# Performance work log

Measured on AMD Instinct MI355X. Metric: run time of the kernel, lower is better.

Reference implementation:

```python
import jax, jax.numpy as jnp
import numpy as np

N_HEAD = 8
D_MODEL = 512


def setup_inputs() -> dict:
    key = jax.random.key(0)
    ks = jax.random.split(key, 9)
    B, S, D, H = 4, 1024, D_MODEL, N_HEAD
    s = 1.0 / np.sqrt(D)
    return {
        "x": jax.random.normal(ks[0], (B, S, D), dtype=jnp.float32),
        "Wq": jax.random.normal(ks[1], (D, H * D), dtype=jnp.float32) * s,
        "bq": jnp.zeros((H * D,), jnp.float32),
        "Wk": jax.random.normal(ks[2], (D, H * D), dtype=jnp.float32) * s,
        "bk": jnp.zeros((H * D,), jnp.float32),
        "Wv": jax.random.normal(ks[3], (D, H * D), dtype=jnp.float32) * s,
        "bv": jnp.zeros((H * D,), jnp.float32),
        "Wo": jax.random.normal(ks[4], (H * D, D), dtype=jnp.float32) * (1.0 / np.sqrt(H * D)),
        "bo": jnp.zeros((D,), jnp.float32),
    }


def reference(x, Wq, bq, Wk, bk, Wv, bv, Wo, bo):
    B, S, D = x.shape
    H = N_HEAD
    # QKV projections, split into heads: [B, S, H, D] (each head uses full d_model)
    q = (x @ Wq + bq).reshape(B, S, H, D)
    k = (x @ Wk + bk).reshape(B, S, H, D)
    v = (x @ Wv + bv).reshape(B, S, H, D)
    # scores: [H, B, Sq, Sk], scaled by 1/d_model (scale=d_model in original)
    scores = jnp.einsum("bqhd,bkhd->hbqk", q, k) / D
    attn = jax.nn.softmax(scores, axis=-1)
    # context: [B, Sq, H, D] -> concat heads -> output projection
    ctx = jnp.einsum("hbqk,bkhd->bqhd", attn, v).reshape(B, S, H * D)
    out = ctx @ Wo + bo
    # attn returned as [(H*B), Sq, Sk] matching torch head-major layout
    return out, attn.reshape(H * B, S, S)
```

## Files before the change

### kernel.cpp

```cpp
#include <hip/hip_runtime.h>
#include <hip/hip_bf16.h>


typedef unsigned short u16;
typedef __attribute__((ext_vector_type(8))) short short8;
typedef __attribute__((ext_vector_type(4))) float f32x4;
typedef __attribute__((ext_vector_type(2))) unsigned int u32x2;

#define BK 32

__device__ __forceinline__ u16 f2bf(float f) {
    union { float f; unsigned u; } v; v.f = f;
    unsigned u = v.u;
    u += 0x7fffu + ((u >> 16) & 1u);
    return (u16)(u >> 16);
}

__device__ __forceinline__ void gl2lds16(const void* g, void* l) {
    __builtin_amdgcn_global_load_lds(
        (const __attribute__((address_space(1))) void*)g,
        (__attribute__((address_space(3))) void*)l, 16, 0, 0);
}

template<int MF, int NF, bool AF32, bool OUTF32, bool ROWBIAS, bool PIPE, bool DUALN>
__global__ __launch_bounds__(256, 4)
void gemm_bt(const void* __restrict__ Ap, int lda, long long sAh, long long sAb,
             const u16* __restrict__ Bp, int ldb, long long sBh, long long sBb,
             void* __restrict__ Cp, int ldc, long long sCh, long long sCb,
             int K, const float* __restrict__ bias, long long sbias,
             float scale, int nb,
             int nsplit, void* __restrict__ Cp2, const float* __restrict__ bias2)
{
    static_assert(!(PIPE && AF32), "PIPE path assumes bf16 A staging");
    constexpr int BMt = MF * 32, BNt = NF * 32;
    constexpr int AW = AF32 ? 2 * BK : BK;
    constexpr int NBUF = PIPE ? 3 : 1;
    constexpr int LPT = BMt / 64 + BNt / 64;
    __shared__ __attribute__((aligned(16))) u16 Alds[NBUF][BMt][AW];
    __shared__ __attribute__((aligned(16))) u16 Blds[NBUF][BNt][BK];

    int bx = blockIdx.x, by = blockIdx.y, bz = blockIdx.z;
    {
        const int gx = gridDim.x, gy = gridDim.y;
        const int nwg = gx * gy * (int)gridDim.z;
        const int wgid = bx + gx * (by + gy * bz);
        const int xcd = wgid & 7, lp = wgid >> 3;
        const int q = nwg >> 3, r = nwg & 7;
        int nid = (xcd < r ? xcd * (q + 1) : r * (q + 1) + (xcd - r) * q) + lp;
        bx = nid % gx; nid /= gx; by = nid % gy; bz = nid / gy;
    }

    const int zh = bz / nb, zb = bz % nb;
    const int m0 = by * BMt;
    const int n0 = bx * BNt;

    const int tid  = threadIdx.x;
    const int lane = tid & 63;
    const int wave = tid >> 6;
    const int wm = (wave >> 1) * (MF * 16);
    const int wn = (wave & 1) * (NF * 16);

    const float* Afp = (const float*)Ap + (long long)zh * sAh + (long long)zb * sAb;
    const u16*   Abf = (const u16*)Ap + (long long)zh * sAh + (long long)zb * sAb;
    const u16*   Bbf = Bp + (long long)zh * sBh + (long long)zb * sBb;

    void* Csel = Cp;
    const float* bsel = bias;
    int nC = n0;
    if (DUALN && n0 >= nsplit) { Csel = Cp2; bsel = bias2; nC = n0 - nsplit; }

    f32x4 acc[MF][NF] = {};

    auto stage = [&](int buf, int kt) {
        if (AF32) {
            #pragma unroll
            for (int i = 0; i < BMt / 32; ++i) {
                int idx = i * 256 + tid;
                int row = idx >> 3;
                int c   = idx & 7;
                int cs  = c ^ (row & 7);
                gl2lds16(Afp + (long long)(m0 + row) * lda + kt + (cs << 2),
                         (u16*)&Alds[buf][0][0] + idx * 8);
            }
        } else {
            #pragma unroll
            for (int i = 0; i < BMt / 64; ++i) {
                int idx = i * 256 + tid;
                int row = idx >> 2;
                int kq  = (idx & 3) << 3;
                gl2lds16(Abf + (long long)(m0 + row) * lda + (kt + kq),
                         &Alds[buf][row][kq]);
            }
        }
        #pragma unroll
        for (int i = 0; i < BNt / 64; ++i) {
            int idx = i * 256 + tid;
            int row = idx >> 2;
            int kq  = (idx & 3) << 3;
            gl2lds16(Bbf + (long long)(n0 + row) * ldb + (kt + kq),
                     &Blds[buf][row][kq]);
        }
    };

    auto compute = [&](int buf) {
        const int kq = (lane >> 4) << 3;
        const int fr = lane & 15;
        short8 af[MF], bfr[NF];
        if (AF32) {
            const int c0 = (lane >> 4) << 1;
            #pragma unroll
            for (int im = 0; im < MF; ++im) {
                int row = wm + im * 16 + fr;
                int s   = row & 7;
                const float* ar = (const float*)&Alds[buf][row][0];
                f32x4 lo = *(const f32x4*)(ar + (((c0    ) ^ s) << 2));
                f32x4 hi = *(const f32x4*)(ar + (((c0 + 1) ^ s) << 2));
                union { short8 v; __hip_bfloat162 h[4]; } a;
                a.h[0] = __float22bfloat162_rn(make_float2(lo.x, lo.y));
                a.h[1] = __float22bfloat162_rn(make_float2(lo.z, lo.w));
                a.h[2] = __float22bfloat162_rn(make_float2(hi.x, hi.y));
                a.h[3] = __float22bfloat162_rn(make_float2(hi.z, hi.w));
                af[im] = a.v;
            }
        } else {
            #pragma unroll
            for (int im = 0; im < MF; ++im)
                af[im] = *(const short8*)(&Alds[buf][wm + im * 16 + fr][kq]);
        }
        #pragma unroll
        for (int in = 0; in < NF; ++in)
            bfr[in] = *(const short8*)(&Blds[buf][wn + in * 16 + fr][kq]);
        #pragma unroll
        for (int im = 0; im < MF; ++im)
            #pragma unroll
            for (int in = 0; in < NF; ++in)
                acc[im][in] = __builtin_amdgcn_mfma_f32_16x16x32_bf16(
                    af[im], bfr[in], acc[im][in], 0, 0, 0);
    };

    const int nt = K / BK;
    if (PIPE) {
        stage(0, 0);
        stage(1, BK);
        for (int t = 0; t < nt; ++t) {
            if (t < nt - 1) {
                if constexpr (LPT == 4)
                    asm volatile("s_waitcnt vmcnt(4)" ::: "memory");
                else if constexpr (LPT == 3)
                    asm volatile("s_waitcnt vmcnt(3)" ::: "memory");
                else if constexpr (LPT == 2)
                    asm volatile("s_waitcnt vmcnt(2)" ::: "memory");
                else
                    asm volatile("s_waitcnt vmcnt(0)" ::: "memory");
            } else {
                asm volatile("s_waitcnt vmcnt(0)" ::: "memory");
            }
            __builtin_amdgcn_s_barrier();
            __builtin_amdgcn_sched_barrier(0);
            const int nx = t + 2;
            if (nx < nt) stage(nx - nx / 3 * 3, nx * BK);
            compute(t - t / 3 * 3);
        }
        __builtin_amdgcn_s_barrier();
    } else {
        for (int t = 0; t < nt; ++t) {
            __syncthreads();
            stage(0, t * BK);
            __syncthreads();
            compute(0);
        }
    }

    float* Cfp = (float*)Csel + (long long)zh * sCh + (long long)zb * sCb;
    u16*   Cbf = (u16*)Csel + (long long)zh * sCh + (long long)zb * sCb;
    const float* biasp = bsel ? bsel + (long long)zh * sbias : nullptr;
    const int rb  = (lane >> 4) << 2;
    const int col = lane & 15;
    #pragma unroll
    for (int im = 0; im < MF; ++im) {
        #pragma unroll
        for (int r = 0; r < 4; ++r) {
            int row = m0 + wm + im * 16 + rb + r;
            float rbias = (biasp && ROWBIAS) ? biasp[row] : 0.0f;
            #pragma unroll
            for (int in = 0; in < NF; ++in) {
                int cc = nC + wn + in * 16 + col;
                float v = acc[im][in][r] * scale;
                if (biasp) v += ROWBIAS ? rbias : biasp[cc];
                if (OUTF32) Cfp[(long long)row * ldc + cc] = v;
                else        Cbf[(long long)row * ldc + cc] = f2bf(v);
            }
        }
    }
}

__global__ __launch_bounds__(256)
void softmax_kernel(float* __restrict__ attn)
{
    const long long row = blockIdx.x;
    float* p = attn + row * 1024;
    const int tid  = threadIdx.x;
    const int lane = tid & 63;
    const int wave = tid >> 6;
    __shared__ float red[8];

    f32x4 v = *(f32x4*)(p + tid * 4);
    float mx = fmaxf(fmaxf(v.x, v.y), fmaxf(v.z, v.w));
    #pragma unroll
    for (int off = 1; off < 64; off <<= 1)
        mx = fmaxf(mx, __shfl_xor(mx, off, 64));
    if (lane == 0) red[wave] = mx;
    __syncthreads();
    mx = fmaxf(fmaxf(red[0], red[1]), fmaxf(red[2], red[3]));

    v.x = __expf(v.x - mx);
    v.y = __expf(v.y - mx);
    v.z = __expf(v.z - mx);
    v.w = __expf(v.w - mx);
    float s = v.x + v.y + v.z + v.w;
    #pragma unroll
    for (int off = 1; off < 64; off <<= 1)
        s += __shfl_xor(s, off, 64);
    if (lane == 0) red[4 + wave] = s;
    __syncthreads();
    s = red[4] + red[5] + red[6] + red[7];
    float inv = 1.0f / s;
    v.x *= inv; v.y *= inv; v.z *= inv; v.w *= inv;
    *(f32x4*)(p + tid * 4) = v;
}

__global__ __launch_bounds__(256)
void cvt_kernel(const float* __restrict__ in, u16* __restrict__ out)
{
    long long i = (long long)blockIdx.x * 256 + threadIdx.x;
    f32x4 v = *(const f32x4*)(in + i * 4);
    u32x2 p;
    p.x = (unsigned)f2bf(v.x) | ((unsigned)f2bf(v.y) << 16);
    p.y = (unsigned)f2bf(v.z) | ((unsigned)f2bf(v.w) << 16);
    *(u32x2*)(out + i * 4) = p;
}

__global__ __launch_bounds__(256)
void wtrans_kernel(const float* __restrict__ in, u16* __restrict__ out, int R, int C)
{
    __shared__ __attribute__((aligned(16))) u16 t[64][72];
    const int r0 = blockIdx.y * 64, c0 = blockIdx.x * 64;
    const int tid = threadIdx.x;
    const int lr = tid >> 4;
    const int lc = (tid & 15) << 2;
    #pragma unroll
    for (int j = 0; j < 4; ++j) {
        int rr = lr + j * 16;
        f32x4 v = *(const f32x4*)(in + (long long)(r0 + rr) * C + c0 + lc);
        u32x2 p;
        p.x = (unsigned)f2bf(v.x) | ((unsigned)f2bf(v.y) << 16);
        p.y = (unsigned)f2bf(v.z) | ((unsigned)f2bf(v.w) << 16);
        *(u32x2*)(&t[rr][lc]) = p;
    }
    __syncthreads();
    const int oc = tid >> 2;
    const int rs = (tid & 3) << 4;
    union { short8 v; u16 e[8]; } a, b;
    #pragma unroll
    for (int j = 0; j < 8; ++j) a.e[j] = t[rs + j][oc];
    #pragma unroll
    for (int j = 0; j < 8; ++j) b.e[j] = t[rs + 8 + j][oc];
    u16* o = out + (long long)(c0 + oc) * R + r0 + rs;
    *(short8*)o = a.v;
    *(short8*)(o + 8) = b.v;
}

extern "C" void kernel_launch(void* const* d_in, const int* in_sizes, int n_in,
                              void* d_out, int out_size, void* d_ws, size_t ws_size,
                              hipStream_t stream)
{
    const float* x  = (const float*)d_in[0];
    const float* Wq = (const float*)d_in[1];
    const float* bq = (const float*)d_in[2];
    const float* Wk = (const float*)d_in[3];
    const float* bk = (const float*)d_in[4];
    const float* Wv = (const float*)d_in[5];
    const float* bv = (const float*)d_in[6];
    const float* Wo = (const float*)d_in[7];
    const float* bo = (const float*)d_in[8];

    const int B = 4, S = 1024, D = 512, H = 8;
    const int HD = H * D;
    const int BS = B * S;

    float* out  = (float*)d_out;
    float* attn = out + (long long)BS * D;

    u16* xb   = (u16*)d_ws;
    u16* WqT  = xb  + (long long)BS * D;
    u16* WkT  = WqT + (long long)HD * D;
    u16* WvT  = WkT + (long long)HD * D;
    u16* WoT  = WvT + (long long)HD * D;
    u16* buf1 = WoT + (long long)D * HD;
    u16* buf2 = buf1 + (long long)BS * HD;

    dim3 blk(256);

    cvt_kernel<<<dim3(BS * D / 1024), blk, 0, stream>>>(x, xb);
    wtrans_kernel<<<dim3(HD / 64, D / 64), blk, 0, stream>>>(Wq, WqT, D, HD);
    wtrans_kernel<<<dim3(HD / 64, D / 64), blk, 0, stream>>>(Wk, WkT, D, HD);
    wtrans_kernel<<<dim3(HD / 64, D / 64), blk, 0, stream>>>(Wv, WvT, D, HD);
    wtrans_kernel<<<dim3(D / 64, HD / 64), blk, 0, stream>>>(Wo, WoT, HD, D);

    {
        dim3 g(2 * HD / 128, BS / 128, 1);
        gemm_bt<4,4,false,false,false,true,true><<<g, blk, 0, stream>>>(
            xb, D, 0, 0, WqT, D, 0, 0, buf1, HD, 0, 0, D, bq, 0, 1.0f, 1,
            HD, buf2, bk);
    }
    {
        dim3 g(S / 128, S / 128, H * B);
        gemm_bt<4,4,false,true,false,true,false><<<g, blk, 0, stream>>>(
            buf1, HD, D, (long long)S * HD,
            buf2, HD, D, (long long)S * HD,
            attn, S, (long long)B * S * S, (long long)S * S,
            D, nullptr, 0, 1.0f / (float)D, B,
            1 << 30, nullptr, nullptr);
    }
    softmax_kernel<<<dim3(H * B * S), blk, 0, stream>>>(attn);
    {
        dim3 g(S / 128, D / 128, H * B);
        gemm_bt<4,4,false,false,true,true,false><<<g, blk, 0, stream>>>(
            WvT, D, (long long)D * D, 0,
            xb, D, 0, (long long)S * D,
            buf1, S, (long long)B * D * S, (long long)D * S,
            D, bv, D, 1.0f, B,
            1 << 30, nullptr, nullptr);
    }
    {
        dim3 g(D / 128, S / 128, H * B);
        gemm_bt<4,4,true,false,false,false,false><<<g, blk, 0, stream>>>(
            attn, S, (long long)B * S * S, (long long)S * S,
            buf1, S, (long long)B * D * S, (long long)D * S,
            buf2, HD, D, (long long)S * HD,
            S, nullptr, 0, 1.0f, B,
            1 << 30, nullptr, nullptr);
    }
    {
        dim3 g(D / 64, BS / 64, 1);
        gemm_bt<2,2,false,true,false,true,false><<<g, blk, 0, stream>>>(
            buf2, HD, 0, 0, WoT, HD, 0, 0, out, D, 0, 0, HD, bo, 0, 1.0f, 1,
            1 << 30, nullptr, nullptr);
    }
}
```

Measured before the change: 479.6 us.

## Register-prefetch f32 A tiles in non-pipelined GEMM path

New measurement: 518.2 us. 8.0% more time.

```diff
diff --git a/kernel.cpp b/kernel.cpp
--- a/kernel.cpp
+++ b/kernel.cpp
@@ -72,25 +72,13 @@
     f32x4 acc[MF][NF] = {};
 
     auto stage = [&](int buf, int kt) {
-        if (AF32) {
-            #pragma unroll
-            for (int i = 0; i < BMt / 32; ++i) {
-                int idx = i * 256 + tid;
-                int row = idx >> 3;
-                int c   = idx & 7;
-                int cs  = c ^ (row & 7);
-                gl2lds16(Afp + (long long)(m0 + row) * lda + kt + (cs << 2),
-                         (u16*)&Alds[buf][0][0] + idx * 8);
-            }
-        } else {
-            #pragma unroll
-            for (int i = 0; i < BMt / 64; ++i) {
-                int idx = i * 256 + tid;
-                int row = idx >> 2;
-                int kq  = (idx & 3) << 3;
-                gl2lds16(Abf + (long long)(m0 + row) * lda + (kt + kq),
-                         &Alds[buf][row][kq]);
-            }
+        #pragma unroll
+        for (int i = 0; i < BMt / 64; ++i) {
+            int idx = i * 256 + tid;
+            int row = idx >> 2;
+            int kq  = (idx & 3) << 3;
+            gl2lds16(Abf + (long long)(m0 + row) * lda + (kt + kq),
+                     &Alds[buf][row][kq]);
         }
         #pragma unroll
         for (int i = 0; i < BNt / 64; ++i) {
@@ -162,6 +150,43 @@
             compute(t - t / 3 * 3);
         }
         __builtin_amdgcn_s_barrier();
+    } else if (AF32) {
+        f32x4 pa[BMt / 32];
+        f32x4 pb[BNt / 64];
+        auto load_regs = [&](int kt) {
+            #pragma unroll
+            for (int i = 0; i < BMt / 32; ++i) {
+                int idx = i * 256 + tid, row = idx >> 3, c = idx & 7;
+                pa[i] = *(const f32x4*)(Afp + (long long)(m0 + row) * lda
+                                        + kt + (c << 2));
+            }
+            #pragma unroll
+            for (int i = 0; i < BNt / 64; ++i) {
+                int idx = i * 256 + tid, row = idx >> 2, kq = (idx & 3) << 3;
+                pb[i] = *(const f32x4*)(Bbf + (long long)(n0 + row) * ldb
+                                        + (kt + kq));
+            }
+        };
+        auto write_lds = [&]() {
+            #pragma unroll
+            for (int i = 0; i < BMt / 32; ++i) {
+                int idx = i * 256 + tid, row = idx >> 3, c = idx & 7;
+                *(f32x4*)(&Alds[0][row][(c ^ (row & 7)) << 3]) = pa[i];
+            }
+            #pragma unroll
+            for (int i = 0; i < BNt / 64; ++i) {
+                int idx = i * 256 + tid, row = idx >> 2, kq = (idx & 3) << 3;
+                *(f32x4*)(&Blds[0][row][kq]) = pb[i];
+            }
+        };
+        load_regs(0);
+        for (int t = 0; t < nt; ++t) {
+            __syncthreads();
+            write_lds();
+            if (t + 1 < nt) load_regs((t + 1) * BK);
+            __syncthreads();
+            compute(0);
+        }
     } else {
         for (int t = 0; t < nt; ++t) {
             __syncthreads();
```
